# Performance work log

Measured on AMD Instinct MI355X. Metric: run time of the kernel, lower is better.

Reference implementation:

```python
import jax, jax.numpy as jnp
import numpy as np

Lx, Ly, D, P = 4, 5, 4, 2
DEPTH = 5
TAU = 0.1
N = Lx * Ly
B = 64


def setup_inputs() -> dict:
    key = jax.random.key(0)
    k1, k2, k3 = jax.random.split(key, 3)
    # PEPS site tensors: [Lx, Ly, phys, up, down, left, right]; boundary bonds sliced to dim 1 at use.
    peps = jax.random.normal(k1, (Lx, Ly, P, D, D, D, D), dtype=jnp.float32) * 0.5
    # Two-site Trotter gate: expm(-tau * h) for a random symmetric two-body term h (4x4).
    h = jax.random.normal(k2, (4, 4), dtype=jnp.float32)
    h = 0.5 * (h + h.T)
    w, v = jnp.linalg.eigh(h)
    gate = (v * jnp.exp(-TAU * w)) @ v.T  # [4,4]
    x = jax.random.randint(k3, (B, N), 0, 2, dtype=jnp.int32)
    return {"x": x, "peps": peps, "gate": gate}


def _slice_boundary(site, i, j):
    # site: [p, u, d, l, r]; open boundary -> bond dim 1 on lattice edges
    if i == 0:
        site = site[:, :1]
    if i == Lx - 1:
        site = site[:, :, :1]
    if j == 0:
        site = site[:, :, :, :1]
    if j == Ly - 1:
        site = site[..., :1]
    return site


def _peps_statevector(peps):
    # Exact contraction of the open-boundary PEPS to the full 2^N statevector.
    rows = []
    for i in range(Lx):
        T = jnp.ones((1, 1, 1, 1), dtype=peps.dtype)  # [Pphys, Uup, Ddown, l]
        for j in range(Ly):
            s = _slice_boundary(peps[i, j], i, j)
            T = jnp.einsum('PUDl,pudlr->PpUuDdr', T, s)
            Pn, p, U, u, Dn, d, r = T.shape
            T = T.reshape(Pn * p, U * u, Dn * d, r)
        rows.append(T[..., 0])  # [2^Ly, up_bonds, down_bonds]
    S = jnp.ones((1, 1), dtype=peps.dtype)  # [Pphys, down_bonds]
    for row in rows:
        S = jnp.einsum('PU,QUD->PQD', S, row)
        a, b, c = S.shape
        S = S.reshape(a * b, c)
    return S[:, 0]  # [2^N]


def _apply_gate(psi, g, a, b):
    # g: [2,2,2,2] = gate[o1,o2,i1,i2]; psi: (2,)*N
    out = jnp.tensordot(g, psi, axes=([2, 3], [a, b]))
    return jnp.moveaxis(out, (0, 1), (a, b))


def _bonds():
    horiz = [((i, j), (i, j + 1)) for i in range(Lx) for j in range(Ly - 1)]
    vert = [((i, j), (i + 1, j)) for i in range(Lx - 1) for j in range(Ly)]
    return horiz + vert


def reference(x, peps, gate):
    psi = _peps_statevector(peps).reshape((2,) * N)
    g = gate.reshape(2, 2, 2, 2)
    bonds = _bonds()
    for _ in range(DEPTH):
        for (i1, j1), (i2, j2) in bonds:
            psi = _apply_gate(psi, g, i1 * Ly + j1, i2 * Ly + j2)
    psi = psi.reshape(-1)
    pw = 2 ** jnp.arange(N - 1, -1, -1, dtype=jnp.int32)
    idx = (x * pw).sum(axis=1)
    return psi[idx]  # [B] amplitudes
```

## Files before the change

### kernel.cpp

```cpp
#include <hip/hip_runtime.h>


#define PAD(i) ((i) + (((i) >> 4) << 2))
#define PIDX(i,j,p,u,d,l,r) (((((((i)*5+(j))*2+(p))*4+(u))*4+(d))*4+(l))*4+(r))

static constexpr int COL0  = 0;
static constexpr int COL1  = 4096;
static constexpr int COL2  = COL1 + 1048576;
static constexpr int COL3  = COL2 + 1048576;
static constexpr int COL4  = COL3 + 1048576;
static constexpr int M01TO = COL4 + 4096;
static constexpr int M34TO = M01TO + 65536;
static constexpr int T12TO = M34TO + 65536;
static constexpr int PSIO  = T12TO + 1048576;

__global__ __launch_bounds__(256) void k_build_cols(const float* __restrict__ peps,
                                                    float* __restrict__ ws) {
  __shared__ float p01[4096], p23[4096];
  int bid = blockIdx.x, t = threadIdx.x;
  if (bid < 384) {
    int col = 1 + (bid >> 7);
    int part = bid & 127;
#pragma unroll
    for (int k = 0; k < 16; ++k) {
      int e = k * 256 + t;
      int r12 = e & 15, l12 = (e >> 4) & 15, d2 = (e >> 8) & 3, p = e >> 10;
      int l1 = l12 >> 2, l2 = l12 & 3, r1 = r12 >> 2, r2 = r12 & 3;
      float s01 = 0.f, s23 = 0.f;
#pragma unroll
      for (int d = 0; d < 4; ++d) {
        s01 += peps[PIDX(0, col, (p >> 1), 0, d, l1, r1)] *
               peps[PIDX(1, col, (p & 1), d, d2, l2, r2)];
        s23 += peps[PIDX(2, col, (p >> 1), d2, d, l1, r1)] *
               peps[PIDX(3, col, (p & 1), d, 0, l2, r2)];
      }
      p01[e] = s01;
      p23[e] = s23;
    }
    __syncthreads();
    const int coloffs[3] = {COL1, COL2, COL3};
    float* out = ws + coloffs[col - 1];
#pragma unroll
    for (int k = 0; k < 8; ++k) {
      int eq = part * 8192 + (k * 256 + t) * 4;
      int r34b = eq & 15;
      int r12 = (eq >> 4) & 15, l34 = (eq >> 8) & 15, l12 = (eq >> 12) & 15;
      int p = eq >> 16;
      int pa = p >> 2, pb = p & 3;
      float4 acc = {0.f, 0.f, 0.f, 0.f};
#pragma unroll
      for (int d2 = 0; d2 < 4; ++d2) {
        float a01 = p01[((((pa * 4 + d2) << 4) | l12) << 4) | r12];
        const float4 b4 =
            *(const float4*)&p23[((((pb * 4 + d2) << 4) | l34) << 4) | r34b];
        acc.x += a01 * b4.x;
        acc.y += a01 * b4.y;
        acc.z += a01 * b4.z;
        acc.w += a01 * b4.w;
      }
      *(float4*)&out[eq] = acc;
    }
  } else {
    int col = (bid == 384) ? 0 : 4;
    const int lsh = (col == 0) ? 0 : 2;
    const int rsh = (col == 4) ? 0 : 2;
    const int ldim = 1 << lsh, rdim = 1 << rsh;
    const int LLB = 2 * lsh, RRB = 2 * rsh;
    const int LL = 1 << LLB, RR = 1 << RRB;
    int n12 = (LL * RR) << 4;
    for (int e = t; e < n12; e += 256) {
      int r12 = e & (RR - 1);
      int l12 = (e >> RRB) & (LL - 1);
      int d2 = (e >> (RRB + LLB)) & 3;
      int p = e >> (RRB + LLB + 2);
      int l1 = l12 >> lsh, l2 = l12 & (ldim - 1);
      int r1 = r12 >> rsh, r2 = r12 & (rdim - 1);
      float s01 = 0.f, s23 = 0.f;
      for (int d = 0; d < 4; ++d) {
        s01 += peps[PIDX(0, col, (p >> 1), 0, d, l1, r1)] *
               peps[PIDX(1, col, (p & 1), d, d2, l2, r2)];
        s23 += peps[PIDX(2, col, (p >> 1), d2, d, l1, r1)] *
               peps[PIDX(3, col, (p & 1), d, 0, l2, r2)];
      }
      p01[e] = s01;
      p23[e] = s23;
    }
    __syncthreads();
    const int LB = 2 * LLB, RB = 2 * RRB;
    int total = 16 << (LB + RB);
    float* out = ws + ((col == 0) ? COL0 : COL4);
    for (int e = t; e < total; e += 256) {
      int r = e & ((1 << RB) - 1);
      int l = (e >> RB) & ((1 << LB) - 1);
      int p = e >> (RB + LB);
      int r34 = r & (RR - 1), r12 = r >> RRB;
      int l34 = l & (LL - 1), l12 = l >> LLB;
      int pa = p >> 2, pb = p & 3;
      float s = 0.f;
      for (int d2 = 0; d2 < 4; ++d2) {
        s += p01[((((pa * 4 + d2) << LLB) | l12) << RRB) | r12] *
             p23[((((pb * 4 + d2) << LLB) | l34) << RRB) | r34];
      }
      out[e] = s;
    }
  }
}

__global__ __launch_bounds__(256) void k_small(const float* __restrict__ ws,
                                               float* __restrict__ m01,
                                               float* __restrict__ m34t) {
  __shared__ float c3buf[4112], c4buf[4112];
  int t = threadIdx.x;
  if (blockIdx.x < 64) {
    int c1 = blockIdx.x >> 2, q = blockIdx.x & 3;
    int r2l = t & 63, c0g = t >> 6;
    int R2 = q * 64 + r2l;
    const float* col0 = ws + COL0;
    const float* col1 = ws + COL1;
    float a0 = 0.f, a1 = 0.f, a2 = 0.f, a3 = 0.f;
    for (int R1 = 0; R1 < 256; ++R1) {
      float bv = col1[(c1 * 256 + R1) * 256 + R2];
      a0 += col0[(c0g * 4 + 0) * 256 + R1] * bv;
      a1 += col0[(c0g * 4 + 1) * 256 + R1] * bv;
      a2 += col0[(c0g * 4 + 2) * 256 + R1] * bv;
      a3 += col0[(c0g * 4 + 3) * 256 + R1] * bv;
    }
    m01[((c0g * 4 + 0) * 16 + c1) * 256 + R2] = a0;
    m01[((c0g * 4 + 1) * 16 + c1) * 256 + R2] = a1;
    m01[((c0g * 4 + 2) * 16 + c1) * 256 + R2] = a2;
    m01[((c0g * 4 + 3) * 16 + c1) * 256 + R2] = a3;
  } else {
    int L3 = blockIdx.x - 64;
    const float* col3 = ws + COL3;
    const float* col4 = ws + COL4;
    for (int e = t; e < 4096; e += 256) {
      c4buf[(e >> 8) * 257 + (e & 255)] = col4[e];
      c3buf[(e >> 8) * 257 + (e & 255)] =
          col3[(e >> 8) * 65536 + L3 * 256 + (e & 255)];
    }
    __syncthreads();
    int c3 = t >> 4, c4 = t & 15;
    float acc = 0.f;
    for (int B = 0; B < 256; ++B)
      acc += c3buf[c3 * 257 + B] * c4buf[c4 * 257 + B];
    m34t[L3 * 256 + t] = acc;
  }
}

__global__ __launch_bounds__(256) void k_t012(const float* __restrict__ m01,
                                              const float* __restrict__ col2,
                                              float* __restrict__ t012) {
  __shared__ float A[4096];
  int t = threadIdx.x;
  int c2 = blockIdx.x & 15, tg = blockIdx.x >> 4;
#pragma unroll
  for (int k = 0; k < 4; ++k)
    *(float4*)&A[(k * 256 + t) * 4] =
        *(const float4*)&m01[tg * 4096 + (k * 256 + t) * 4];
  __syncthreads();
  float acc[16] = {};
  for (int R2 = 0; R2 < 256; R2 += 4) {
    float b0 = col2[c2 * 65536 + (R2 + 0) * 256 + t];
    float b1 = col2[c2 * 65536 + (R2 + 1) * 256 + t];
    float b2 = col2[c2 * 65536 + (R2 + 2) * 256 + t];
    float b3 = col2[c2 * 65536 + (R2 + 3) * 256 + t];
#pragma unroll
    for (int i = 0; i < 16; ++i) {
      float4 a4 = *(const float4*)&A[i * 256 + R2];
      acc[i] += a4.x * b0 + a4.y * b1 + a4.z * b2 + a4.w * b3;
    }
  }
#pragma unroll
  for (int i = 0; i < 16; ++i)
    t012[c2 * 65536 + (tg * 16 + i) * 256 + t] = acc[i];
}

__global__ __launch_bounds__(256) void k_psi0(const float* __restrict__ t012,
                                              const float* __restrict__ m34t,
                                              float* __restrict__ psi) {
  __shared__ float A[4096];
  __shared__ float S[4112];
  int t = threadIdx.x;
  int tg = blockIdx.x;
#pragma unroll
  for (int i = 0; i < 16; ++i)
    A[i * 256 + t] = t012[i * 65536 + tg * 256 + t];
  __syncthreads();
  float acc[16] = {};
  for (int L3 = 0; L3 < 256; L3 += 4) {
    float b0 = m34t[(L3 + 0) * 256 + t];
    float b1 = m34t[(L3 + 1) * 256 + t];
    float b2 = m34t[(L3 + 2) * 256 + t];
    float b3 = m34t[(L3 + 3) * 256 + t];
#pragma unroll
    for (int i = 0; i < 16; ++i) {
      float4 a4 = *(const float4*)&A[i * 256 + L3];
      acc[i] += a4.x * b0 + a4.y * b1 + a4.z * b2 + a4.w * b3;
    }
  }
#pragma unroll
  for (int i = 0; i < 16; ++i) S[i * 257 + t] = acc[i];
  __syncthreads();
  int c3 = t >> 4, c2 = t & 15;
  int base = c3 * 65536 + (tg >> 4) * 256 + (tg & 15) * 16 + c2;
#pragma unroll
  for (int v = 0; v < 16; ++v)
    psi[base + v * 4096] = S[c2 * 257 + c3 * 16 + v];
}

template <int NB, int HI, int LO>
__device__ __forceinline__ void gate2(float* x, const float* __restrict__ g) {
  constexpr int H = 1 << HI, L = 1 << LO, N = 1 << NB;
#pragma unroll
  for (int o = 0; o < N; ++o) {
    if (o & (H | L)) continue;
    float v0 = x[o], v1 = x[o + L], v2 = x[o + H], v3 = x[o + H + L];
    x[o]         = g[0]  * v0 + g[1]  * v1 + g[2]  * v2 + g[3]  * v3;
    x[o + L]     = g[4]  * v0 + g[5]  * v1 + g[6]  * v2 + g[7]  * v3;
    x[o + H]     = g[8]  * v0 + g[9]  * v1 + g[10] * v2 + g[11] * v3;
    x[o + H + L] = g[12] * v0 + g[13] * v1 + g[14] * v2 + g[15] * v3;
  }
}

template <int ST>
__device__ __forceinline__ void vxf(float* s, const float* __restrict__ g, int b) {
  float x[16];
#pragma unroll
  for (int m = 0; m < 16; ++m) x[m] = s[PAD(b + m * ST)];
  gate2<4, 3, 2>(x, g);
  gate2<4, 2, 1>(x, g);
  gate2<4, 1, 0>(x, g);
#pragma unroll
  for (int m = 0; m < 16; ++m) s[PAD(b + m * ST)] = x[m];
}

template <int B2, int B1, int B0>
__device__ __forceinline__ void bondpair(float* s, const float* __restrict__ g,
                                         int t) {
  constexpr int MASK = (1 << B2) | (1 << B1) | (1 << B0);
  int b = 0, rem = t;
#pragma unroll
  for (int p = 0; p < 12; ++p) {
    if (!((MASK >> p) & 1)) {
      b |= (rem & 1) << p;
      rem >>= 1;
    }
  }
  float x[8];
#pragma unroll
  for (int m = 0; m < 8; ++m) {
    int off = ((m >> 2) & 1) * (1 << B2) + ((m >> 1) & 1) * (1 << B1) +
              (m & 1) * (1 << B0);
    x[m] = s[PAD(b + off)];
  }
  gate2<3, 2, 1>(x, g);
  gate2<3, 1, 0>(x, g);
#pragma unroll
  for (int m = 0; m < 8; ++m) {
    int off = ((m >> 2) & 1) * (1 << B2) + ((m >> 1) & 1) * (1 << B1) +
              (m & 1) * (1 << B0);
    s[PAD(b + off)] = x[m];
  }
}

__global__ __launch_bounds__(512) void k_P1(float* __restrict__ psi,
                                            const float* __restrict__ gate) {
  __shared__ float s[5120];
  float g[16];
#pragma unroll
  for (int i = 0; i < 16; ++i) g[i] = gate[i];
  int t = threadIdx.x;
  int o = blockIdx.x;
#pragma unroll
  for (int i = 0; i < 2; ++i) {
    int f = (i * 512 + t) * 4;
    *(float4*)(s + PAD(f)) = *(const float4*)(psi + o * 4096 + f);
  }
  __syncthreads();
  bondpair<8, 4, 0>(s, g, t);
  __syncthreads();
  bondpair<9, 5, 1>(s, g, t);
  __syncthreads();
  bondpair<10, 6, 2>(s, g, t);
  __syncthreads();
  bondpair<11, 7, 3>(s, g, t);
  __syncthreads();
  if (t < 256) vxf<256>(s, g, t);
  __syncthreads();
  if (t < 256) vxf<16>(s, g, ((t >> 4) << 8) | (t & 15));
  __syncthreads();
#pragma unroll
  for (int i = 0; i < 2; ++i) {
    int f = (i * 512 + t) * 4;
    *(float4*)(psi + o * 4096 + f) = *(const float4*)(s + PAD(f));
  }
}

template <bool LAST>
__global__ __launch_bounds__(512) void k_P2(float* __restrict__ psi,
                                            const float* __restrict__ gate,
                                            const int* __restrict__ x,
                                            float* __restrict__ out) {
  __shared__ float s[5120];
  float g[16];
#pragma unroll
  for (int i = 0; i < 16; ++i) g[i] = gate[i];
  int t = threadIdx.x;
  int o = blockIdx.x;
#pragma unroll
  for (int i = 0; i < 2; ++i) {
    int f = (i * 512 + t) * 4;
    int addr = (f >> 8) * 65536 + ((f >> 4) & 15) * 4096 + o * 16 + (f & 15);
    *(float4*)(s + PAD(f)) = *(const float4*)(psi + addr);
  }
  __syncthreads();
  bondpair<0, 8, 4>(s, g, t);
  __syncthreads();
  bondpair<1, 9, 5>(s, g, t);
  __syncthreads();
  bondpair<2, 10, 6>(s, g, t);
  __syncthreads();
  bondpair<3, 11, 7>(s, g, t);
  __syncthreads();
  if (t < 256) vxf<1>(s, g, t * 16);
  __syncthreads();
  if (t < 256) vxf<256>(s, g, t);
  __syncthreads();
  if (t < 256) vxf<16>(s, g, ((t >> 4) << 8) | (t & 15));
  __syncthreads();
  if (LAST) {
    if (t < 64) {
      int idx = 0;
#pragma unroll
      for (int q = 0; q < 20; ++q) {
        int i = q / 5, j = q % 5;
        int pos = (j == 0) ? (11 - i)
                 : (j == 1) ? (7 - i)
                 : (j == 2) ? (3 - i)
                 : (j == 3) ? (19 - i)
                            : (15 - i);
        idx |= x[t * 20 + q] << pos;
      }
      if (((idx >> 4) & 255) == o) {
        int local = ((idx >> 16) & 15) * 256 + ((idx >> 12) & 15) * 16 +
                    (idx & 15);
        out[t] = s[PAD(local)];
      }
    }
  } else {
#pragma unroll
    for (int i = 0; i < 2; ++i) {
      int f = (i * 512 + t) * 4;
      int addr = (f >> 8) * 65536 + ((f >> 4) & 15) * 4096 + o * 16 + (f & 15);
      *(float4*)(psi + addr) = *(const float4*)(s + PAD(f));
    }
  }
}

extern "C" void kernel_launch(void* const* d_in, const int* in_sizes, int n_in,
                              void* d_out, int out_size, void* d_ws, size_t ws_size,
                              hipStream_t stream) {
  const int* x = (const int*)d_in[0];
  const float* peps = (const float*)d_in[1];
  const float* gate = (const float*)d_in[2];
  float* ws = (float*)d_ws;
  float* psi = ws + PSIO;
  float* out = (float*)d_out;

  k_build_cols<<<386, 256, 0, stream>>>(peps, ws);
  k_small<<<320, 256, 0, stream>>>(ws, ws + M01TO, ws + M34TO);
  k_t012<<<256, 256, 0, stream>>>(ws + M01TO, ws + COL2, ws + T12TO);
  k_psi0<<<256, 256, 0, stream>>>(ws + T12TO, ws + M34TO, psi);

  for (int it = 0; it < 5; ++it) {
    k_P1<<<256, 512, 0, stream>>>(psi, gate);
    if (it < 4)
      k_P2<false><<<256, 512, 0, stream>>>(psi, gate, x, out);
    else
      k_P2<true><<<256, 512, 0, stream>>>(psi, gate, x, out);
  }
}
```

Before: 214.2 us.

## Fuse all stages into one cooperative persistent kernel with grid syncs

After: 590.5 us. +175.6%, slower.

```diff
diff --git a/kernel.cpp b/kernel.cpp
--- a/kernel.cpp
+++ b/kernel.cpp
@@ -1,4 +1,7 @@
 #include <hip/hip_runtime.h>
+#include <hip/hip_cooperative_groups.h>
+
+namespace cg = cooperative_groups;
 
 
 #define PAD(i) ((i) + (((i) >> 4) << 2))
@@ -14,16 +17,81 @@
 static constexpr int T12TO = M34TO + 65536;
 static constexpr int PSIO  = T12TO + 1048576;
 
-__global__ __launch_bounds__(256) void k_build_cols(const float* __restrict__ peps,
-                                                    float* __restrict__ ws) {
-  __shared__ float p01[4096], p23[4096];
-  int bid = blockIdx.x, t = threadIdx.x;
-  if (bid < 384) {
-    int col = 1 + (bid >> 7);
-    int part = bid & 127;
-#pragma unroll
-    for (int k = 0; k < 16; ++k) {
-      int e = k * 256 + t;
+template <int NB, int HI, int LO>
+__device__ __forceinline__ void gate2(float* x, const float* __restrict__ g) {
+  constexpr int H = 1 << HI, L = 1 << LO, N = 1 << NB;
+#pragma unroll
+  for (int o = 0; o < N; ++o) {
+    if (o & (H | L)) continue;
+    float v0 = x[o], v1 = x[o + L], v2 = x[o + H], v3 = x[o + H + L];
+    x[o]         = g[0]  * v0 + g[1]  * v1 + g[2]  * v2 + g[3]  * v3;
+    x[o + L]     = g[4]  * v0 + g[5]  * v1 + g[6]  * v2 + g[7]  * v3;
+    x[o + H]     = g[8]  * v0 + g[9]  * v1 + g[10] * v2 + g[11] * v3;
+    x[o + H + L] = g[12] * v0 + g[13] * v1 + g[14] * v2 + g[15] * v3;
+  }
+}
+
+template <int ST>
+__device__ __forceinline__ void vxf(float* s, const float* __restrict__ g, int b) {
+  float x[16];
+#pragma unroll
+  for (int m = 0; m < 16; ++m) x[m] = s[PAD(b + m * ST)];
+  gate2<4, 3, 2>(x, g);
+  gate2<4, 2, 1>(x, g);
+  gate2<4, 1, 0>(x, g);
+#pragma unroll
+  for (int m = 0; m < 16; ++m) s[PAD(b + m * ST)] = x[m];
+}
+
+template <int B2, int B1, int B0>
+__device__ __forceinline__ void bondpair(float* s, const float* __restrict__ g,
+                                         int t) {
+  constexpr int MASK = (1 << B2) | (1 << B1) | (1 << B0);
+  int b = 0, rem = t;
+#pragma unroll
+  for (int p = 0; p < 12; ++p) {
+    if (!((MASK >> p) & 1)) {
+      b |= (rem & 1) << p;
+      rem >>= 1;
+    }
+  }
+  float x[8];
+#pragma unroll
+  for (int m = 0; m < 8; ++m) {
+    int off = ((m >> 2) & 1) * (1 << B2) + ((m >> 1) & 1) * (1 << B1) +
+              (m & 1) * (1 << B0);
+    x[m] = s[PAD(b + off)];
+  }
+  gate2<3, 2, 1>(x, g);
+  gate2<3, 1, 0>(x, g);
+#pragma unroll
+  for (int m = 0; m < 8; ++m) {
+    int off = ((m >> 2) & 1) * (1 << B2) + ((m >> 1) & 1) * (1 << B1) +
+              (m & 1) * (1 << B0);
+    s[PAD(b + off)] = x[m];
+  }
+}
+
+__global__ __launch_bounds__(512, 2) void k_fused(const float* __restrict__ peps,
+                                                  const int* __restrict__ x,
+                                                  const float* __restrict__ gate,
+                                                  float* __restrict__ ws,
+                                                  float* __restrict__ out) {
+  cg::grid_group gg = cg::this_grid();
+  __shared__ float sm[8224];
+  const int t = threadIdx.x;
+  const int b = blockIdx.x;
+  const int r3 = t & 255, half = t >> 8;
+  float* psi = ws + PSIO;
+
+  if (b < 192) {
+    float* p01 = sm;
+    float* p23 = sm + 4096;
+    int col = 1 + (b >> 6);
+    int pb = b & 63;
+#pragma unroll
+    for (int k = 0; k < 8; ++k) {
+      int e = k * 512 + t;
       int r12 = e & 15, l12 = (e >> 4) & 15, d2 = (e >> 8) & 3, p = e >> 10;
       int l1 = l12 >> 2, l2 = l12 & 3, r1 = r12 >> 2, r2 = r12 & 3;
       float s01 = 0.f, s23 = 0.f;
@@ -39,36 +107,42 @@
     }
     __syncthreads();
     const int coloffs[3] = {COL1, COL2, COL3};
-    float* out = ws + coloffs[col - 1];
-#pragma unroll
-    for (int k = 0; k < 8; ++k) {
-      int eq = part * 8192 + (k * 256 + t) * 4;
-      int r34b = eq & 15;
-      int r12 = (eq >> 4) & 15, l34 = (eq >> 8) & 15, l12 = (eq >> 12) & 15;
-      int p = eq >> 16;
-      int pa = p >> 2, pb = p & 3;
-      float4 acc = {0.f, 0.f, 0.f, 0.f};
-#pragma unroll
-      for (int d2 = 0; d2 < 4; ++d2) {
-        float a01 = p01[((((pa * 4 + d2) << 4) | l12) << 4) | r12];
-        const float4 b4 =
-            *(const float4*)&p23[((((pb * 4 + d2) << 4) | l34) << 4) | r34b];
-        acc.x += a01 * b4.x;
-        acc.y += a01 * b4.y;
-        acc.z += a01 * b4.z;
-        acc.w += a01 * b4.w;
-      }
-      *(float4*)&out[eq] = acc;
-    }
-  } else {
-    int col = (bid == 384) ? 0 : 4;
+    float* outc = ws + coloffs[col - 1];
+#pragma unroll
+    for (int pp = 0; pp < 2; ++pp) {
+      int part = pb * 2 + pp;
+#pragma unroll
+      for (int k = 0; k < 4; ++k) {
+        int eq = part * 8192 + (k * 512 + t) * 4;
+        int r34b = eq & 15;
+        int r12 = (eq >> 4) & 15, l34 = (eq >> 8) & 15, l12 = (eq >> 12) & 15;
+        int p = eq >> 16;
+        int pa = p >> 2, pbv = p & 3;
+        float4 acc = {0.f, 0.f, 0.f, 0.f};
+#pragma unroll
+        for (int d2 = 0; d2 < 4; ++d2) {
+          float a01 = p01[((((pa * 4 + d2) << 4) | l12) << 4) | r12];
+          const float4 b4 =
+              *(const float4*)&p23[((((pbv * 4 + d2) << 4) | l34) << 4) | r34b];
+          acc.x += a01 * b4.x;
+          acc.y += a01 * b4.y;
+          acc.z += a01 * b4.z;
+          acc.w += a01 * b4.w;
+        }
+        *(float4*)&outc[eq] = acc;
+      }
+    }
+  } else if (b < 194) {
+    float* p01 = sm;
+    float* p23 = sm + 4096;
+    int col = (b == 192) ? 0 : 4;
     const int lsh = (col == 0) ? 0 : 2;
     const int rsh = (col == 4) ? 0 : 2;
     const int ldim = 1 << lsh, rdim = 1 << rsh;
     const int LLB = 2 * lsh, RRB = 2 * rsh;
     const int LL = 1 << LLB, RR = 1 << RRB;
     int n12 = (LL * RR) << 4;
-    for (int e = t; e < n12; e += 256) {
+    for (int e = t; e < n12; e += 512) {
       int r12 = e & (RR - 1);
       int l12 = (e >> RRB) & (LL - 1);
       int d2 = (e >> (RRB + LLB)) & 3;
@@ -88,271 +162,213 @@
     __syncthreads();
     const int LB = 2 * LLB, RB = 2 * RRB;
     int total = 16 << (LB + RB);
-    float* out = ws + ((col == 0) ? COL0 : COL4);
-    for (int e = t; e < total; e += 256) {
+    float* outc = ws + ((col == 0) ? COL0 : COL4);
+    for (int e = t; e < total; e += 512) {
       int r = e & ((1 << RB) - 1);
       int l = (e >> RB) & ((1 << LB) - 1);
       int p = e >> (RB + LB);
       int r34 = r & (RR - 1), r12 = r >> RRB;
       int l34 = l & (LL - 1), l12 = l >> LLB;
-      int pa = p >> 2, pb = p & 3;
-      float s = 0.f;
+      int pa = p >> 2, pbv = p & 3;
+      float sacc = 0.f;
       for (int d2 = 0; d2 < 4; ++d2) {
-        s += p01[((((pa * 4 + d2) << LLB) | l12) << RRB) | r12] *
-             p23[((((pb * 4 + d2) << LLB) | l34) << RRB) | r34];
-      }
-      out[e] = s;
-    }
-  }
-}
-
-__global__ __launch_bounds__(256) void k_small(const float* __restrict__ ws,
-                                               float* __restrict__ m01,
-                                               float* __restrict__ m34t) {
-  __shared__ float c3buf[4112], c4buf[4112];
-  int t = threadIdx.x;
-  if (blockIdx.x < 64) {
-    int c1 = blockIdx.x >> 2, q = blockIdx.x & 3;
-    int r2l = t & 63, c0g = t >> 6;
-    int R2 = q * 64 + r2l;
-    const float* col0 = ws + COL0;
-    const float* col1 = ws + COL1;
-    float a0 = 0.f, a1 = 0.f, a2 = 0.f, a3 = 0.f;
-    for (int R1 = 0; R1 < 256; ++R1) {
-      float bv = col1[(c1 * 256 + R1) * 256 + R2];
-      a0 += col0[(c0g * 4 + 0) * 256 + R1] * bv;
-      a1 += col0[(c0g * 4 + 1) * 256 + R1] * bv;
-      a2 += col0[(c0g * 4 + 2) * 256 + R1] * bv;
-      a3 += col0[(c0g * 4 + 3) * 256 + R1] * bv;
-    }
-    m01[((c0g * 4 + 0) * 16 + c1) * 256 + R2] = a0;
-    m01[((c0g * 4 + 1) * 16 + c1) * 256 + R2] = a1;
-    m01[((c0g * 4 + 2) * 16 + c1) * 256 + R2] = a2;
-    m01[((c0g * 4 + 3) * 16 + c1) * 256 + R2] = a3;
-  } else {
-    int L3 = blockIdx.x - 64;
+        sacc += p01[((((pa * 4 + d2) << LLB) | l12) << RRB) | r12] *
+                p23[((((pbv * 4 + d2) << LLB) | l34) << RRB) | r34];
+      }
+      outc[e] = sacc;
+    }
+  }
+  gg.sync();
+
+  {
+    float* c3buf = sm;
+    float* c4buf = sm + 4112;
     const float* col3 = ws + COL3;
     const float* col4 = ws + COL4;
-    for (int e = t; e < 4096; e += 256) {
-      c4buf[(e >> 8) * 257 + (e & 255)] = col4[e];
-      c3buf[(e >> 8) * 257 + (e & 255)] =
-          col3[(e >> 8) * 65536 + L3 * 256 + (e & 255)];
-    }
-    __syncthreads();
-    int c3 = t >> 4, c4 = t & 15;
-    float acc = 0.f;
-    for (int B = 0; B < 256; ++B)
-      acc += c3buf[c3 * 257 + B] * c4buf[c4 * 257 + B];
-    m34t[L3 * 256 + t] = acc;
-  }
-}
-
-__global__ __launch_bounds__(256) void k_t012(const float* __restrict__ m01,
-                                              const float* __restrict__ col2,
-                                              float* __restrict__ t012) {
-  __shared__ float A[4096];
-  int t = threadIdx.x;
-  int c2 = blockIdx.x & 15, tg = blockIdx.x >> 4;
-#pragma unroll
-  for (int k = 0; k < 4; ++k)
-    *(float4*)&A[(k * 256 + t) * 4] =
-        *(const float4*)&m01[tg * 4096 + (k * 256 + t) * 4];
-  __syncthreads();
-  float acc[16] = {};
-  for (int R2 = 0; R2 < 256; R2 += 4) {
-    float b0 = col2[c2 * 65536 + (R2 + 0) * 256 + t];
-    float b1 = col2[c2 * 65536 + (R2 + 1) * 256 + t];
-    float b2 = col2[c2 * 65536 + (R2 + 2) * 256 + t];
-    float b3 = col2[c2 * 65536 + (R2 + 3) * 256 + t];
-#pragma unroll
-    for (int i = 0; i < 16; ++i) {
-      float4 a4 = *(const float4*)&A[i * 256 + R2];
-      acc[i] += a4.x * b0 + a4.y * b1 + a4.z * b2 + a4.w * b3;
-    }
-  }
-#pragma unroll
-  for (int i = 0; i < 16; ++i)
-    t012[c2 * 65536 + (tg * 16 + i) * 256 + t] = acc[i];
-}
-
-__global__ __launch_bounds__(256) void k_psi0(const float* __restrict__ t012,
-                                              const float* __restrict__ m34t,
-                                              float* __restrict__ psi) {
-  __shared__ float A[4096];
-  __shared__ float S[4112];
-  int t = threadIdx.x;
-  int tg = blockIdx.x;
-#pragma unroll
-  for (int i = 0; i < 16; ++i)
-    A[i * 256 + t] = t012[i * 65536 + tg * 256 + t];
-  __syncthreads();
-  float acc[16] = {};
-  for (int L3 = 0; L3 < 256; L3 += 4) {
-    float b0 = m34t[(L3 + 0) * 256 + t];
-    float b1 = m34t[(L3 + 1) * 256 + t];
-    float b2 = m34t[(L3 + 2) * 256 + t];
-    float b3 = m34t[(L3 + 3) * 256 + t];
-#pragma unroll
-    for (int i = 0; i < 16; ++i) {
-      float4 a4 = *(const float4*)&A[i * 256 + L3];
-      acc[i] += a4.x * b0 + a4.y * b1 + a4.z * b2 + a4.w * b3;
-    }
-  }
-#pragma unroll
-  for (int i = 0; i < 16; ++i) S[i * 257 + t] = acc[i];
-  __syncthreads();
-  int c3 = t >> 4, c2 = t & 15;
-  int base = c3 * 65536 + (tg >> 4) * 256 + (tg & 15) * 16 + c2;
-#pragma unroll
-  for (int v = 0; v < 16; ++v)
-    psi[base + v * 4096] = S[c2 * 257 + c3 * 16 + v];
-}
-
-template <int NB, int HI, int LO>
-__device__ __forceinline__ void gate2(float* x, const float* __restrict__ g) {
-  constexpr int H = 1 << HI, L = 1 << LO, N = 1 << NB;
-#pragma unroll
-  for (int o = 0; o < N; ++o) {
-    if (o & (H | L)) continue;
-    float v0 = x[o], v1 = x[o + L], v2 = x[o + H], v3 = x[o + H + L];
-    x[o]         = g[0]  * v0 + g[1]  * v1 + g[2]  * v2 + g[3]  * v3;
-    x[o + L]     = g[4]  * v0 + g[5]  * v1 + g[6]  * v2 + g[7]  * v3;
-    x[o + H]     = g[8]  * v0 + g[9]  * v1 + g[10] * v2 + g[11] * v3;
-    x[o + H + L] = g[12] * v0 + g[13] * v1 + g[14] * v2 + g[15] * v3;
-  }
-}
-
-template <int ST>
-__device__ __forceinline__ void vxf(float* s, const float* __restrict__ g, int b) {
-  float x[16];
-#pragma unroll
-  for (int m = 0; m < 16; ++m) x[m] = s[PAD(b + m * ST)];
-  gate2<4, 3, 2>(x, g);
-  gate2<4, 2, 1>(x, g);
-  gate2<4, 1, 0>(x, g);
-#pragma unroll
-  for (int m = 0; m < 16; ++m) s[PAD(b + m * ST)] = x[m];
-}
-
-template <int B2, int B1, int B0>
-__device__ __forceinline__ void bondpair(float* s, const float* __restrict__ g,
-                                         int t) {
-  constexpr int MASK = (1 << B2) | (1 << B1) | (1 << B0);
-  int b = 0, rem = t;
-#pragma unroll
-  for (int p = 0; p < 12; ++p) {
-    if (!((MASK >> p) & 1)) {
-      b |= (rem & 1) << p;
-      rem >>= 1;
-    }
-  }
-  float x[8];
-#pragma unroll
-  for (int m = 0; m < 8; ++m) {
-    int off = ((m >> 2) & 1) * (1 << B2) + ((m >> 1) & 1) * (1 << B1) +
-              (m & 1) * (1 << B0);
-    x[m] = s[PAD(b + off)];
-  }
-  gate2<3, 2, 1>(x, g);
-  gate2<3, 1, 0>(x, g);
-#pragma unroll
-  for (int m = 0; m < 8; ++m) {
-    int off = ((m >> 2) & 1) * (1 << B2) + ((m >> 1) & 1) * (1 << B1) +
-              (m & 1) * (1 << B0);
-    s[PAD(b + off)] = x[m];
-  }
-}
-
-__global__ __launch_bounds__(512) void k_P1(float* __restrict__ psi,
-                                            const float* __restrict__ gate) {
-  __shared__ float s[5120];
+    const int L3 = b;
+    if (t < 256) {
+      for (int e = t; e < 4096; e += 256) {
+        c4buf[(e >> 8) * 257 + (e & 255)] = col4[e];
+        c3buf[(e >> 8) * 257 + (e & 255)] =
+            col3[(e >> 8) * 65536 + L3 * 256 + (e & 255)];
+      }
+    } else if (b < 64) {
+      int tt = t - 256;
+      int c1 = b >> 2, q = b & 3;
+      int r2l = tt & 63, c0g = tt >> 6;
+      int R2 = q * 64 + r2l;
+      const float* col0 = ws + COL0;
+      const float* col1 = ws + COL1;
+      float a0 = 0.f, a1 = 0.f, a2 = 0.f, a3 = 0.f;
+      for (int R1 = 0; R1 < 256; ++R1) {
+        float bv = col1[(c1 * 256 + R1) * 256 + R2];
+        a0 += col0[(c0g * 4 + 0) * 256 + R1] * bv;
+        a1 += col0[(c0g * 4 + 1) * 256 + R1] * bv;
+        a2 += col0[(c0g * 4 + 2) * 256 + R1] * bv;
+        a3 += col0[(c0g * 4 + 3) * 256 + R1] * bv;
+      }
+      float* m01 = ws + M01TO;
+      m01[((c0g * 4 + 0) * 16 + c1) * 256 + R2] = a0;
+      m01[((c0g * 4 + 1) * 16 + c1) * 256 + R2] = a1;
+      m01[((c0g * 4 + 2) * 16 + c1) * 256 + R2] = a2;
+      m01[((c0g * 4 + 3) * 16 + c1) * 256 + R2] = a3;
+    }
+    __syncthreads();
+    if (t < 256) {
+      int c3 = t >> 4, c4 = t & 15;
+      float acc = 0.f;
+      for (int B = 0; B < 256; ++B)
+        acc += c3buf[c3 * 257 + B] * c4buf[c4 * 257 + B];
+      float* m34t = ws + M34TO;
+      m34t[L3 * 256 + t] = acc;
+    }
+  }
+  gg.sync();
+
+  {
+    float* A = sm;
+    const float* m01 = ws + M01TO;
+    const float* col2 = ws + COL2;
+    float* t012p = ws + T12TO;
+    int c2 = b & 15, tg = b >> 4;
+#pragma unroll
+    for (int k = 0; k < 2; ++k)
+      *(float4*)&A[(k * 512 + t) * 4] =
+          *(const float4*)&m01[tg * 4096 + (k * 512 + t) * 4];
+    __syncthreads();
+    float acc[8] = {};
+    for (int R2 = 0; R2 < 256; R2 += 4) {
+      float b0 = col2[c2 * 65536 + (R2 + 0) * 256 + r3];
+      float b1 = col2[c2 * 65536 + (R2 + 1) * 256 + r3];
+      float b2 = col2[c2 * 65536 + (R2 + 2) * 256 + r3];
+      float b3 = col2[c2 * 65536 + (R2 + 3) * 256 + r3];
+#pragma unroll
+      for (int i = 0; i < 8; ++i) {
+        float4 a4 = *(const float4*)&A[(half * 8 + i) * 256 + R2];
+        acc[i] += a4.x * b0 + a4.y * b1 + a4.z * b2 + a4.w * b3;
+      }
+    }
+#pragma unroll
+    for (int i = 0; i < 8; ++i)
+      t012p[c2 * 65536 + (tg * 16 + half * 8 + i) * 256 + r3] = acc[i];
+  }
+  gg.sync();
+
+  {
+    float* A = sm;
+    float* S = sm + 4096;
+    const float* t012p = ws + T12TO;
+    const float* m34t = ws + M34TO;
+    int tg = b;
+#pragma unroll
+    for (int i = 0; i < 8; ++i)
+      A[(half * 8 + i) * 256 + r3] =
+          t012p[(half * 8 + i) * 65536 + tg * 256 + r3];
+    __syncthreads();
+    float acc[8] = {};
+    for (int L3 = 0; L3 < 256; L3 += 4) {
+      float b0 = m34t[(L3 + 0) * 256 + r3];
+      float b1 = m34t[(L3 + 1) * 256 + r3];
+      float b2 = m34t[(L3 + 2) * 256 + r3];
+      float b3 = m34t[(L3 + 3) * 256 + r3];
+#pragma unroll
+      for (int i = 0; i < 8; ++i) {
+        float4 a4 = *(const float4*)&A[(half * 8 + i) * 256 + L3];
+        acc[i] += a4.x * b0 + a4.y * b1 + a4.z * b2 + a4.w * b3;
+      }
+    }
+#pragma unroll
+    for (int i = 0; i < 8; ++i) S[(half * 8 + i) * 257 + r3] = acc[i];
+    __syncthreads();
+    int c3 = r3 >> 4, c2 = r3 & 15;
+    int base = c3 * 65536 + (tg >> 4) * 256 + (tg & 15) * 16 + c2;
+#pragma unroll
+    for (int vv = 0; vv < 8; ++vv) {
+      int v = half * 8 + vv;
+      psi[base + v * 4096] = S[c2 * 257 + c3 * 16 + v];
+    }
+  }
+  gg.sync();
+
   float g[16];
 #pragma unroll
   for (int i = 0; i < 16; ++i) g[i] = gate[i];
-  int t = threadIdx.x;
-  int o = blockIdx.x;
-#pragma unroll
-  for (int i = 0; i < 2; ++i) {
-    int f = (i * 512 + t) * 4;
-    *(float4*)(s + PAD(f)) = *(const float4*)(psi + o * 4096 + f);
-  }
-  __syncthreads();
-  bondpair<8, 4, 0>(s, g, t);
-  __syncthreads();
-  bondpair<9, 5, 1>(s, g, t);
-  __syncthreads();
-  bondpair<10, 6, 2>(s, g, t);
-  __syncthreads();
-  bondpair<11, 7, 3>(s, g, t);
-  __syncthreads();
-  if (t < 256) vxf<256>(s, g, t);
-  __syncthreads();
-  if (t < 256) vxf<16>(s, g, ((t >> 4) << 8) | (t & 15));
-  __syncthreads();
-#pragma unroll
-  for (int i = 0; i < 2; ++i) {
-    int f = (i * 512 + t) * 4;
-    *(float4*)(psi + o * 4096 + f) = *(const float4*)(s + PAD(f));
-  }
-}
-
-template <bool LAST>
-__global__ __launch_bounds__(512) void k_P2(float* __restrict__ psi,
-                                            const float* __restrict__ gate,
-                                            const int* __restrict__ x,
-                                            float* __restrict__ out) {
-  __shared__ float s[5120];
-  float g[16];
-#pragma unroll
-  for (int i = 0; i < 16; ++i) g[i] = gate[i];
-  int t = threadIdx.x;
-  int o = blockIdx.x;
-#pragma unroll
-  for (int i = 0; i < 2; ++i) {
-    int f = (i * 512 + t) * 4;
-    int addr = (f >> 8) * 65536 + ((f >> 4) & 15) * 4096 + o * 16 + (f & 15);
-    *(float4*)(s + PAD(f)) = *(const float4*)(psi + addr);
-  }
-  __syncthreads();
-  bondpair<0, 8, 4>(s, g, t);
-  __syncthreads();
-  bondpair<1, 9, 5>(s, g, t);
-  __syncthreads();
-  bondpair<2, 10, 6>(s, g, t);
-  __syncthreads();
-  bondpair<3, 11, 7>(s, g, t);
-  __syncthreads();
-  if (t < 256) vxf<1>(s, g, t * 16);
-  __syncthreads();
-  if (t < 256) vxf<256>(s, g, t);
-  __syncthreads();
-  if (t < 256) vxf<16>(s, g, ((t >> 4) << 8) | (t & 15));
-  __syncthreads();
-  if (LAST) {
-    if (t < 64) {
-      int idx = 0;
-#pragma unroll
-      for (int q = 0; q < 20; ++q) {
-        int i = q / 5, j = q % 5;
-        int pos = (j == 0) ? (11 - i)
-                 : (j == 1) ? (7 - i)
-                 : (j == 2) ? (3 - i)
-                 : (j == 3) ? (19 - i)
-                            : (15 - i);
-        idx |= x[t * 20 + q] << pos;
-      }
-      if (((idx >> 4) & 255) == o) {
-        int local = ((idx >> 16) & 15) * 256 + ((idx >> 12) & 15) * 16 +
-                    (idx & 15);
-        out[t] = s[PAD(local)];
-      }
-    }
-  } else {
+  float* s = sm;
+
+  for (int it = 0; it < 5; ++it) {
 #pragma unroll
     for (int i = 0; i < 2; ++i) {
       int f = (i * 512 + t) * 4;
-      int addr = (f >> 8) * 65536 + ((f >> 4) & 15) * 4096 + o * 16 + (f & 15);
-      *(float4*)(psi + addr) = *(const float4*)(s + PAD(f));
+      *(float4*)(s + PAD(f)) = *(const float4*)(psi + b * 4096 + f);
+    }
+    __syncthreads();
+    bondpair<8, 4, 0>(s, g, t);
+    __syncthreads();
+    bondpair<9, 5, 1>(s, g, t);
+    __syncthreads();
+    bondpair<10, 6, 2>(s, g, t);
+    __syncthreads();
+    bondpair<11, 7, 3>(s, g, t);
+    __syncthreads();
+    if (t < 256) vxf<256>(s, g, t);
+    __syncthreads();
+    if (t < 256) vxf<16>(s, g, ((t >> 4) << 8) | (t & 15));
+    __syncthreads();
+#pragma unroll
+    for (int i = 0; i < 2; ++i) {
+      int f = (i * 512 + t) * 4;
+      *(float4*)(psi + b * 4096 + f) = *(const float4*)(s + PAD(f));
+    }
+    gg.sync();
+
+#pragma unroll
+    for (int i = 0; i < 2; ++i) {
+      int f = (i * 512 + t) * 4;
+      int addr = (f >> 8) * 65536 + ((f >> 4) & 15) * 4096 + b * 16 + (f & 15);
+      *(float4*)(s + PAD(f)) = *(const float4*)(psi + addr);
+    }
+    __syncthreads();
+    bondpair<0, 8, 4>(s, g, t);
+    __syncthreads();
+    bondpair<1, 9, 5>(s, g, t);
+    __syncthreads();
+    bondpair<2, 10, 6>(s, g, t);
+    __syncthreads();
+    bondpair<3, 11, 7>(s, g, t);
+    __syncthreads();
+    if (t < 256) vxf<1>(s, g, t * 16);
+    __syncthreads();
+    if (t < 256) vxf<256>(s, g, t);
+    __syncthreads();
+    if (t < 256) vxf<16>(s, g, ((t >> 4) << 8) | (t & 15));
+    __syncthreads();
+    if (it == 4) {
+      if (t < 64) {
+        int idx = 0;
+#pragma unroll
+        for (int q = 0; q < 20; ++q) {
+          int i = q / 5, j = q % 5;
+          int pos = (j == 0) ? (11 - i)
+                   : (j == 1) ? (7 - i)
+                   : (j == 2) ? (3 - i)
+                   : (j == 3) ? (19 - i)
+                              : (15 - i);
+          idx |= x[t * 20 + q] << pos;
+        }
+        if (((idx >> 4) & 255) == b) {
+          int local = ((idx >> 16) & 15) * 256 + ((idx >> 12) & 15) * 16 +
+                      (idx & 15);
+          out[t] = s[PAD(local)];
+        }
+      }
+    } else {
+#pragma unroll
+      for (int i = 0; i < 2; ++i) {
+        int f = (i * 512 + t) * 4;
+        int addr = (f >> 8) * 65536 + ((f >> 4) & 15) * 4096 + b * 16 + (f & 15);
+        *(float4*)(psi + addr) = *(const float4*)(s + PAD(f));
+      }
+      gg.sync();
     }
   }
 }
@@ -364,19 +380,9 @@
   const float* peps = (const float*)d_in[1];
   const float* gate = (const float*)d_in[2];
   float* ws = (float*)d_ws;
-  float* psi = ws + PSIO;
   float* out = (float*)d_out;
 
-  k_build_cols<<<386, 256, 0, stream>>>(peps, ws);
-  k_small<<<320, 256, 0, stream>>>(ws, ws + M01TO, ws + M34TO);
-  k_t012<<<256, 256, 0, stream>>>(ws + M01TO, ws + COL2, ws + T12TO);
-  k_psi0<<<256, 256, 0, stream>>>(ws + T12TO, ws + M34TO, psi);
-
-  for (int it = 0; it < 5; ++it) {
-    k_P1<<<256, 512, 0, stream>>>(psi, gate);
-    if (it < 4)
-      k_P2<false><<<256, 512, 0, stream>>>(psi, gate, x, out);
-    else
-      k_P2<true><<<256, 512, 0, stream>>>(psi, gate, x, out);
-  }
-}
+  void* args[] = {(void*)&peps, (void*)&x, (void*)&gate, (void*)&ws, (void*)&out};
+  hipLaunchCooperativeKernel((void*)k_fused, dim3(256), dim3(512), args, 0,
+                             stream);
+}
```

## Fuse gate-phase kernels into one cooperative kernel with grid barriers

Applied to the files above, without the earlier changes.

New measurement: 447.2 us. 109% more time.

```diff
diff --git a/kernel.cpp b/kernel.cpp
--- a/kernel.cpp
+++ b/kernel.cpp
@@ -13,11 +13,13 @@
 static constexpr int M34TO = M01TO + 65536;
 static constexpr int T12TO = M34TO + 65536;
 static constexpr int PSIO  = T12TO + 1048576;
+static constexpr int CNTO  = PSIO + 1048576;
 
 __global__ __launch_bounds__(256) void k_build_cols(const float* __restrict__ peps,
                                                     float* __restrict__ ws) {
   __shared__ float p01[4096], p23[4096];
   int bid = blockIdx.x, t = threadIdx.x;
+  if (bid == 0 && t == 0) ((int*)(ws + CNTO))[0] = 0;
   if (bid < 384) {
     int col = 1 + (bid >> 7);
     int part = bid & 127;
@@ -263,96 +265,109 @@
   }
 }
 
-__global__ __launch_bounds__(512) void k_P1(float* __restrict__ psi,
-                                            const float* __restrict__ gate) {
+__device__ __forceinline__ void gridbar(int* __restrict__ cnt, int tgt) {
+  __syncthreads();
+  if (threadIdx.x == 0) {
+    __threadfence();
+    atomicAdd(cnt, 1);
+    while (__hip_atomic_load(cnt, __ATOMIC_RELAXED,
+                             __HIP_MEMORY_SCOPE_AGENT) < tgt) {
+      __builtin_amdgcn_s_sleep(1);
+    }
+    __threadfence();
+  }
+  __syncthreads();
+}
+
+__global__ __launch_bounds__(512) void k_gates(float* __restrict__ psi,
+                                               const float* __restrict__ gate,
+                                               const int* __restrict__ x,
+                                               float* __restrict__ out,
+                                               int* __restrict__ cnt) {
   __shared__ float s[5120];
   float g[16];
 #pragma unroll
   for (int i = 0; i < 16; ++i) g[i] = gate[i];
-  int t = threadIdx.x;
-  int o = blockIdx.x;
-#pragma unroll
-  for (int i = 0; i < 2; ++i) {
-    int f = (i * 512 + t) * 4;
-    *(float4*)(s + PAD(f)) = *(const float4*)(psi + o * 4096 + f);
-  }
-  __syncthreads();
-  bondpair<8, 4, 0>(s, g, t);
-  __syncthreads();
-  bondpair<9, 5, 1>(s, g, t);
-  __syncthreads();
-  bondpair<10, 6, 2>(s, g, t);
-  __syncthreads();
-  bondpair<11, 7, 3>(s, g, t);
-  __syncthreads();
-  if (t < 256) vxf<256>(s, g, t);
-  __syncthreads();
-  if (t < 256) vxf<16>(s, g, ((t >> 4) << 8) | (t & 15));
-  __syncthreads();
-#pragma unroll
-  for (int i = 0; i < 2; ++i) {
-    int f = (i * 512 + t) * 4;
-    *(float4*)(psi + o * 4096 + f) = *(const float4*)(s + PAD(f));
-  }
-}
-
-template <bool LAST>
-__global__ __launch_bounds__(512) void k_P2(float* __restrict__ psi,
-                                            const float* __restrict__ gate,
-                                            const int* __restrict__ x,
-                                            float* __restrict__ out) {
-  __shared__ float s[5120];
-  float g[16];
-#pragma unroll
-  for (int i = 0; i < 16; ++i) g[i] = gate[i];
-  int t = threadIdx.x;
-  int o = blockIdx.x;
-#pragma unroll
-  for (int i = 0; i < 2; ++i) {
-    int f = (i * 512 + t) * 4;
-    int addr = (f >> 8) * 65536 + ((f >> 4) & 15) * 4096 + o * 16 + (f & 15);
-    *(float4*)(s + PAD(f)) = *(const float4*)(psi + addr);
-  }
-  __syncthreads();
-  bondpair<0, 8, 4>(s, g, t);
-  __syncthreads();
-  bondpair<1, 9, 5>(s, g, t);
-  __syncthreads();
-  bondpair<2, 10, 6>(s, g, t);
-  __syncthreads();
-  bondpair<3, 11, 7>(s, g, t);
-  __syncthreads();
-  if (t < 256) vxf<1>(s, g, t * 16);
-  __syncthreads();
-  if (t < 256) vxf<256>(s, g, t);
-  __syncthreads();
-  if (t < 256) vxf<16>(s, g, ((t >> 4) << 8) | (t & 15));
-  __syncthreads();
-  if (LAST) {
-    if (t < 64) {
-      int idx = 0;
-#pragma unroll
-      for (int q = 0; q < 20; ++q) {
-        int i = q / 5, j = q % 5;
-        int pos = (j == 0) ? (11 - i)
-                 : (j == 1) ? (7 - i)
-                 : (j == 2) ? (3 - i)
-                 : (j == 3) ? (19 - i)
-                            : (15 - i);
-        idx |= x[t * 20 + q] << pos;
-      }
-      if (((idx >> 4) & 255) == o) {
-        int local = ((idx >> 16) & 15) * 256 + ((idx >> 12) & 15) * 16 +
-                    (idx & 15);
-        out[t] = s[PAD(local)];
-      }
-    }
-  } else {
+  const int t = threadIdx.x;
+  const int b = blockIdx.x;
+  int barid = 0;
+
+  for (int it = 0; it < 5; ++it) {
 #pragma unroll
     for (int i = 0; i < 2; ++i) {
       int f = (i * 512 + t) * 4;
-      int addr = (f >> 8) * 65536 + ((f >> 4) & 15) * 4096 + o * 16 + (f & 15);
-      *(float4*)(psi + addr) = *(const float4*)(s + PAD(f));
+      *(float4*)(s + PAD(f)) = *(const float4*)(psi + b * 4096 + f);
+    }
+    __syncthreads();
+    bondpair<8, 4, 0>(s, g, t);
+    __syncthreads();
+    bondpair<9, 5, 1>(s, g, t);
+    __syncthreads();
+    bondpair<10, 6, 2>(s, g, t);
+    __syncthreads();
+    bondpair<11, 7, 3>(s, g, t);
+    __syncthreads();
+    if (t < 256) vxf<256>(s, g, t);
+    __syncthreads();
+    if (t < 256) vxf<16>(s, g, ((t >> 4) << 8) | (t & 15));
+    __syncthreads();
+#pragma unroll
+    for (int i = 0; i < 2; ++i) {
+      int f = (i * 512 + t) * 4;
+      *(float4*)(psi + b * 4096 + f) = *(const float4*)(s + PAD(f));
+    }
+    ++barid;
+    gridbar(cnt, barid * 256);
+
+#pragma unroll
+    for (int i = 0; i < 2; ++i) {
+      int f = (i * 512 + t) * 4;
+      int addr = (f >> 8) * 65536 + ((f >> 4) & 15) * 4096 + b * 16 + (f & 15);
+      *(float4*)(s + PAD(f)) = *(const float4*)(psi + addr);
+    }
+    __syncthreads();
+    bondpair<0, 8, 4>(s, g, t);
+    __syncthreads();
+    bondpair<1, 9, 5>(s, g, t);
+    __syncthreads();
+    bondpair<2, 10, 6>(s, g, t);
+    __syncthreads();
+    bondpair<3, 11, 7>(s, g, t);
+    __syncthreads();
+    if (t < 256) vxf<1>(s, g, t * 16);
+    __syncthreads();
+    if (t < 256) vxf<256>(s, g, t);
+    __syncthreads();
+    if (t < 256) vxf<16>(s, g, ((t >> 4) << 8) | (t & 15));
+    __syncthreads();
+    if (it == 4) {
+      if (t < 64) {
+        int idx = 0;
+#pragma unroll
+        for (int q = 0; q < 20; ++q) {
+          int i = q / 5, j = q % 5;
+          int pos = (j == 0) ? (11 - i)
+                   : (j == 1) ? (7 - i)
+                   : (j == 2) ? (3 - i)
+                   : (j == 3) ? (19 - i)
+                              : (15 - i);
+          idx |= x[t * 20 + q] << pos;
+        }
+        if (((idx >> 4) & 255) == b) {
+          int local = ((idx >> 16) & 15) * 256 + ((idx >> 12) & 15) * 16 +
+                      (idx & 15);
+          out[t] = s[PAD(local)];
+        }
+      }
+    } else {
+#pragma unroll
+      for (int i = 0; i < 2; ++i) {
+        int f = (i * 512 + t) * 4;
+        int addr = (f >> 8) * 65536 + ((f >> 4) & 15) * 4096 + b * 16 + (f & 15);
+        *(float4*)(psi + addr) = *(const float4*)(s + PAD(f));
+      }
+      ++barid;
+      gridbar(cnt, barid * 256);
     }
   }
 }
@@ -366,17 +381,15 @@
   float* ws = (float*)d_ws;
   float* psi = ws + PSIO;
   float* out = (float*)d_out;
+  int* cnt = (int*)(ws + CNTO);
 
   k_build_cols<<<386, 256, 0, stream>>>(peps, ws);
   k_small<<<320, 256, 0, stream>>>(ws, ws + M01TO, ws + M34TO);
   k_t012<<<256, 256, 0, stream>>>(ws + M01TO, ws + COL2, ws + T12TO);
   k_psi0<<<256, 256, 0, stream>>>(ws + T12TO, ws + M34TO, psi);
 
-  for (int it = 0; it < 5; ++it) {
-    k_P1<<<256, 512, 0, stream>>>(psi, gate);
-    if (it < 4)
-      k_P2<false><<<256, 512, 0, stream>>>(psi, gate, x, out);
-    else
-      k_P2<true><<<256, 512, 0, stream>>>(psi, gate, x, out);
-  }
-}
+  void* args[] = {(void*)&psi, (void*)&gate, (void*)&x, (void*)&out,
+                  (void*)&cnt};
+  hipLaunchCooperativeKernel((void*)k_gates, dim3(256), dim3(512), args, 0,
+                             stream);
+}
```
